# Kernel tuning notes

Measured on AMD Instinct MI355X. Metric: run time of the kernel, lower is better.

The kernel has to match this reference:

```python
import jax, jax.numpy as jnp
import numpy as np

N = 50000      # nodes
E = 800000     # edges (before self-loops)
F_IN = 128     # num_node_features
H = 128        # hidden_channels
G = 256        # graphs in batch
T = 4          # num_tasks


def setup_inputs() -> dict:
    key = jax.random.key(0)
    ks = jax.random.split(key, 12)
    x = jax.random.normal(ks[0], (N, F_IN), jnp.float32)
    edge_index = jax.random.randint(ks[1], (2, E), 0, N, dtype=jnp.int64)
    batch = jnp.sort(jax.random.randint(ks[2], (N,), 0, G, dtype=jnp.int64))
    s_in = 1.0 / np.sqrt(F_IN)
    s_h = 1.0 / np.sqrt(H)
    W1 = jax.random.normal(ks[3], (F_IN, H), jnp.float32) * s_in
    b1 = jnp.zeros((H,), jnp.float32)
    W2 = jax.random.normal(ks[4], (H, H), jnp.float32) * s_h
    b2 = jnp.zeros((H,), jnp.float32)
    Wfc = jax.random.normal(ks[5], (H, H), jnp.float32) * s_h
    bfc = jnp.zeros((H,), jnp.float32)
    Wh = jax.random.normal(ks[6], (T, H, 2), jnp.float32) * s_h
    bh = jnp.zeros((T, 2), jnp.float32)
    return {"x": x, "edge_index": edge_index, "batch": batch,
            "W1": W1, "b1": b1, "W2": W2, "b2": b2,
            "Wfc": Wfc, "bfc": bfc, "Wh": Wh, "bh": bh}


def _gcn_layer(x, W, b, src, dst, dinv):
    # GCNConv: out = D^{-1/2}(A+I)D^{-1/2} X W + b  (self-loops already in src/dst)
    h = x @ W                                    # [N, H] dense transform first (fewer edge features)
    coef = dinv[src] * dinv[dst]                 # [E+N] symmetric normalization
    msg = h[src] * coef[:, None]                 # [E+N, H] gathered messages
    out = jax.ops.segment_sum(msg, dst, num_segments=N)
    return out + b


def reference(x, edge_index, batch, W1, b1, W2, b2, Wfc, bfc, Wh, bh):
    loops = jnp.arange(N, dtype=edge_index.dtype)
    src = jnp.concatenate([edge_index[0], loops])  # [E+N]
    dst = jnp.concatenate([edge_index[1], loops])
    deg = jax.ops.segment_sum(jnp.ones_like(dst, dtype=x.dtype), dst, num_segments=N)
    dinv = jax.lax.rsqrt(deg)                      # deg >= 1 due to self-loops

    h = jax.nn.relu(_gcn_layer(x, W1, b1, src, dst, dinv))
    h = jax.nn.relu(_gcn_layer(h, W2, b2, src, dst, dinv))

    # global_mean_pool over batch ids
    sums = jax.ops.segment_sum(h, batch, num_segments=G)          # [G, H]
    cnt = jax.ops.segment_sum(jnp.ones((N,), h.dtype), batch, num_segments=G)
    pooled = sums / jnp.maximum(cnt, 1.0)[:, None]

    z = jax.nn.relu(pooled @ Wfc + bfc)                           # [G, H]
    out = jnp.einsum('gh,thc->tgc', z, Wh) + bh[:, None, :]       # [T, G, 2]
    return out
```

## Files before the change

### kernel.cpp

```cpp
#include <hip/hip_runtime.h>
#include <math.h>

constexpr int N = 50000;
constexpr int E = 800000;
constexpr int F = 128;
constexpr int G = 256;
constexpr int T = 4;

constexpr int BSH   = 5;
constexpr int BNODES= 1 << BSH;
constexpr int NBUCK = (N + BNODES - 1) / BNODES;
constexpr int CHUNK = 2048;
constexpr int NCHUNK= (E + CHUNK - 1) / CHUNK;
constexpr int SSH   = 13;

constexpr int WC_BLKS  = (F * F + 255) / 256;
constexpr int PRE_Z0   = 2 * WC_BLKS;
constexpr int PRE_ZB   = (G * F + 255) / 256;
constexpr int PRE_H0   = PRE_Z0 + PRE_ZB;
constexpr int PRE_BLKS = PRE_H0 + NCHUNK;

constexpr int GB1 = (N + 63) / 64;
constexpr int GCB = GB1 + NBUCK;
constexpr int AGB = N / 16;

typedef __attribute__((ext_vector_type(8))) short short8;
typedef __attribute__((ext_vector_type(4))) float floatx4;

__device__ inline float bf2f(unsigned short u) {
    union { unsigned int i; float f; } v;
    v.i = ((unsigned int)u) << 16;
    return v.f;
}
__device__ inline unsigned short f2bf(float f) {
    union { float f; unsigned int i; } v;
    v.f = f;
    unsigned int r = v.i + 0x7FFF + ((v.i >> 16) & 1);
    return (unsigned short)(r >> 16);
}
__device__ inline unsigned int pack2bf(float a, float b) {
    return (unsigned int)f2bf(a) | ((unsigned int)f2bf(b) << 16);
}

__device__ inline void wcast_one(const float* __restrict__ W,
                                 unsigned short* __restrict__ Whi,
                                 unsigned short* __restrict__ Wlo, int i) {
    if (i >= F * F) return;
    int k = i >> 7, n = i & 127;
    float w = W[i];
    unsigned short hi = f2bf(w);
    unsigned short lo = f2bf(w - bf2f(hi));
    int s = k >> 5, q = (k >> 3) & 3, j = k & 7;
    int idx = (((s * 128 + n) * 4 + q) * 8) + j;
    Whi[idx] = hi;
    Wlo[idx] = lo;
}

__global__ __launch_bounds__(256) void k_pre(const float* __restrict__ W1, const float* __restrict__ W2,
                                             unsigned short* __restrict__ w1h, unsigned short* __restrict__ w1l,
                                             unsigned short* __restrict__ w2h, unsigned short* __restrict__ w2l,
                                             const int* __restrict__ dst, int* __restrict__ cnts,
                                             float* __restrict__ pooled, int* __restrict__ ndeg) {
    __shared__ int h[NBUCK];
    int b = blockIdx.x, t = threadIdx.x;
    if (b < WC_BLKS) {
        wcast_one(W1, w1h, w1l, b * 256 + t);
    } else if (b < 2 * WC_BLKS) {
        wcast_one(W2, w2h, w2l, (b - WC_BLKS) * 256 + t);
    } else if (b < PRE_H0) {
        pooled[(b - PRE_Z0) * 256 + t] = 0.f;
    } else {
        int chunk = b - PRE_H0;
        for (int i = t; i < NBUCK; i += 256) h[i] = 0;
        __syncthreads();
        int base = chunk * CHUNK;
        for (int i = t; i < CHUNK; i += 256) {
            int e = base + i;
            if (e < E) {
                int d = dst[e];
                atomicAdd(&h[d >> BSH], 1);
                atomicAdd(&ndeg[d], 1);
            }
        }
        __syncthreads();
        for (int i = t; i < NBUCK; i += 256) cnts[chunk * NBUCK + i] = h[i];
    }
}

__global__ __launch_bounds__(256) void k_fillb(const int* __restrict__ src,
                                               const int* __restrict__ dst,
                                               const int* __restrict__ cnts,
                                               const int* __restrict__ btot,
                                               int* __restrict__ bucketbase,
                                               unsigned int* __restrict__ staging) {
    __shared__ int bb[NBUCK + 1];
    __shared__ int part[256];
    __shared__ int lofs[NBUCK];
    int chunk = blockIdx.x, t = threadIdx.x;

    constexpr int CH = (NBUCK + 255) / 256;
    int beg = t * CH;
    int end = (beg + CH < NBUCK) ? beg + CH : NBUCK;
    int tot[CH];
    int s = 0;
    for (int i = beg; i < end; ++i) {
        tot[i - beg] = btot[i];
        s += btot[i];
    }
    part[t] = s;
    __syncthreads();
    for (int off = 1; off < 256; off <<= 1) {
        int u = (t >= off) ? part[t - off] : 0;
        __syncthreads();
        part[t] += u;
        __syncthreads();
    }
    int run = (t == 0) ? 0 : part[t - 1];
    for (int i = beg; i < end; ++i) {
        bb[i] = run;
        run += tot[i - beg];
    }
    if (t == 255) bb[NBUCK] = part[255];
    __syncthreads();
    if (chunk == 0)
        for (int i = t; i <= NBUCK; i += 256) bucketbase[i] = bb[i];

    for (int i = t; i < NBUCK; i += 256)
        lofs[i] = bb[i] + cnts[chunk * NBUCK + i];
    __syncthreads();

    int base = chunk * CHUNK;
    for (int i = t; i < CHUNK; i += 256) {
        int e = base + i;
        if (e < E) {
            int d = dst[e];
            int pos = atomicAdd(&lofs[d >> BSH], 1);
            staging[pos] = (unsigned int)src[e] | ((unsigned int)(d & (BNODES - 1)) << 16);
        }
    }
}

__global__ __launch_bounds__(256) void k_passB(const unsigned int* __restrict__ staging,
                                               const int* __restrict__ bucketbase,
                                               int* __restrict__ csr,
                                               int* __restrict__ rowstart) {
    __shared__ unsigned int ent[1024];
    __shared__ int h[BNODES * 8], off_a[BNODES * 8];
    __shared__ int nodebase[BNODES], ndeg[BNODES];
    int b = blockIdx.x, t = threadIdx.x;
    int jb = bucketbase[b], je = bucketbase[b + 1];
    int M = je - jb;
    if (M > 1024) M = 1024;
    if (t < BNODES * 8) h[t] = 0;
    __syncthreads();

    for (int i = t; i < M; i += 256) {
        unsigned int en = staging[jb + i];
        ent[i] = en;
        int key = (((en >> 16) & (BNODES - 1)) << 3) | ((en & 0xFFFFu) >> SSH);
        atomicAdd(&h[key], 1);
    }
    __syncthreads();

    if (t < BNODES) {
        int s = 0;
#pragma unroll
        for (int c = 0; c < 8; ++c) s += h[t * 8 + c];
        ndeg[t] = s;
    }
    __syncthreads();
    if (t == 0) {
        int run = jb;
        for (int k = 0; k < BNODES; ++k) {
            nodebase[k] = run;
            run += ndeg[k];
        }
    }
    __syncthreads();
    if (t < BNODES) {
        int run = nodebase[t];
#pragma unroll
        for (int c = 0; c < 8; ++c) {
            off_a[t * 8 + c] = run;
            run += h[t * 8 + c];
        }
        int node = b * BNODES + t;
        if (node < N) rowstart[node] = nodebase[t];
    }
    if (b == 0 && t == 0) rowstart[N] = E;
    __syncthreads();

    for (int i = t; i < M; i += 256) {
        unsigned int en = ent[i];
        int key = (((en >> 16) & (BNODES - 1)) << 3) | ((en & 0xFFFFu) >> SSH);
        int loc = atomicAdd(&off_a[key], 1);
        csr[loc] = (int)(en & 0xFFFFu);
    }
}

template <bool ABF16>
__device__ __forceinline__ void gemm_body(const void* __restrict__ Ain,
                                          const unsigned short* __restrict__ Wph,
                                          const unsigned short* __restrict__ Wpl,
                                          const int* __restrict__ ndeg,
                                          float* __restrict__ dinvout,
                                          unsigned short* __restrict__ C16,
                                          int row0, int tid,
                                          unsigned short* __restrict__ Albs) {
    if (ABF16) {
        const uint4* A8 = (const uint4*)Ain;
        for (int f = tid; f < 64 * 16; f += 256) {
            int r = f >> 4, kq = f & 15;
            int row = row0 + r;
            uint4 v = make_uint4(0u, 0u, 0u, 0u);
            if (row < N) v = A8[row * 16 + kq];
            *(uint4*)&Albs[r * 136 + kq * 8] = v;
        }
    } else {
        const float4* A4 = (const float4*)Ain;
        for (int f = tid; f < 64 * 32; f += 256) {
            int r = f >> 5, kq = f & 31;
            int row = row0 + r;
            float4 v = make_float4(0.f, 0.f, 0.f, 0.f);
            if (row < N) v = A4[row * 32 + kq];
            ushort4 o;
            o.x = f2bf(v.x); o.y = f2bf(v.y); o.z = f2bf(v.z); o.w = f2bf(v.w);
            *(ushort4*)&Albs[r * 136 + kq * 4] = o;
        }
    }
    __syncthreads();

    int wv = tid >> 6;
    int lane = tid & 63;
    int c16 = lane & 15;
    int q = lane >> 4;
    int m = wv * 16 + c16;

    floatx4 acc[8];
#pragma unroll
    for (int nt = 0; nt < 8; ++nt) acc[nt] = (floatx4){0.f, 0.f, 0.f, 0.f};

    const short8* WH = (const short8*)Wph;
    const short8* WL = (const short8*)Wpl;
#pragma unroll
    for (int s = 0; s < 4; ++s) {
        short8 a = *(const short8*)&Albs[m * 136 + s * 32 + q * 8];
        int wb = s * 512 + c16 * 4 + q;
#pragma unroll
        for (int nt = 0; nt < 8; ++nt) {
            acc[nt] = __builtin_amdgcn_mfma_f32_16x16x32_bf16(a, WH[wb + nt * 64], acc[nt], 0, 0, 0);
            acc[nt] = __builtin_amdgcn_mfma_f32_16x16x32_bf16(a, WL[wb + nt * 64], acc[nt], 0, 0, 0);
        }
    }

    int rbase = row0 + wv * 16 + q * 4;
#pragma unroll
    for (int r = 0; r < 4; ++r) {
        int row = rbase + r;
        if (row < N) {
            float dv = rsqrtf((float)(ndeg[row] + 1));
            if (c16 == 0) dinvout[row] = dv;
#pragma unroll
            for (int nt = 0; nt < 8; ++nt)
                C16[row * 128 + nt * 16 + c16] = f2bf(acc[nt][r] * dv);
        }
    }
}

__global__ __launch_bounds__(256) void k_gemmcol(const float* __restrict__ x,
                                                 const unsigned short* __restrict__ w1h,
                                                 const unsigned short* __restrict__ w1l,
                                                 const int* __restrict__ ndeg,
                                                 float* __restrict__ dinv,
                                                 unsigned short* __restrict__ tmp16,
                                                 int* __restrict__ cnts,
                                                 int* __restrict__ btot) {
    __shared__ __align__(16) unsigned short Albs[64 * 136];
    int b = blockIdx.x, t = threadIdx.x;
    if (b < GB1) {
        gemm_body<false>(x, w1h, w1l, ndeg, dinv, tmp16, b * 64, t, Albs);
        return;
    }
    int j = b - GB1;
    int* part = (int*)Albs;
    int k0 = 2 * t, k1 = 2 * t + 1;
    int v0 = (k0 < NCHUNK) ? cnts[k0 * NBUCK + j] : 0;
    int v1 = (k1 < NCHUNK) ? cnts[k1 * NBUCK + j] : 0;
    int s = v0 + v1;
    part[t] = s;
    __syncthreads();
    for (int off = 1; off < 256; off <<= 1) {
        int u = (t >= off) ? part[t - off] : 0;
        __syncthreads();
        part[t] += u;
        __syncthreads();
    }
    int excl = part[t] - s;
    if (k0 < NCHUNK) cnts[k0 * NBUCK + j] = excl;
    if (k1 < NCHUNK) cnts[k1 * NBUCK + j] = excl + v0;
    if (t == 255) btot[j] = part[255];
}

__device__ inline void add8(const uint4& u, float* acc) {
    union { unsigned int i; float f; } a;
    a.i = u.x << 16;          acc[0] += a.f;
    a.i = u.x & 0xFFFF0000u;  acc[1] += a.f;
    a.i = u.y << 16;          acc[2] += a.f;
    a.i = u.y & 0xFFFF0000u;  acc[3] += a.f;
    a.i = u.z << 16;          acc[4] += a.f;
    a.i = u.z & 0xFFFF0000u;  acc[5] += a.f;
    a.i = u.w << 16;          acc[6] += a.f;
    a.i = u.w & 0xFFFF0000u;  acc[7] += a.f;
}

__device__ inline void fma8(const uint4& u, float c, float* acc) {
    union { unsigned int i; float f; } a;
    a.i = u.x << 16;          acc[0] = fmaf(a.f, c, acc[0]);
    a.i = u.x & 0xFFFF0000u;  acc[1] = fmaf(a.f, c, acc[1]);
    a.i = u.y << 16;          acc[2] = fmaf(a.f, c, acc[2]);
    a.i = u.y & 0xFFFF0000u;  acc[3] = fmaf(a.f, c, acc[3]);
    a.i = u.z << 16;          acc[4] = fmaf(a.f, c, acc[4]);
    a.i = u.z & 0xFFFF0000u;  acc[5] = fmaf(a.f, c, acc[5]);
    a.i = u.w << 16;          acc[6] = fmaf(a.f, c, acc[6]);
    a.i = u.w & 0xFFFF0000u;  acc[7] = fmaf(a.f, c, acc[7]);
}

__device__ __forceinline__ void agg_loop(const uint4* __restrict__ t8l,
                                         const int* __restrict__ csr,
                                         int jb, int je, float* acc) {
    int n8 = (je - jb) >> 3;
    int j = jb;
    if (n8 > 0) {
        int e[8];
#pragma unroll
        for (int k = 0; k < 8; ++k) e[k] = csr[j + k];
        for (int c = 0; c < n8; ++c) {
            uint4 u[8];
#pragma unroll
            for (int k = 0; k < 8; ++k) u[k] = t8l[e[k] * 16];
            j += 8;
            if (c + 1 < n8) {
#pragma unroll
                for (int k = 0; k < 8; ++k) e[k] = csr[j + k];
            }
#pragma unroll
            for (int k = 0; k < 8; ++k) add8(u[k], acc);
        }
    }
    if (j < je) {
        int e[8];
        float msk[8];
#pragma unroll
        for (int k = 0; k < 8; ++k) {
            int idx = j + k;
            e[k] = csr[idx < je ? idx : je - 1];
            msk[k] = (idx < je) ? 1.0f : 0.0f;
        }
        uint4 u[8];
#pragma unroll
        for (int k = 0; k < 8; ++k) u[k] = t8l[e[k] * 16];
#pragma unroll
        for (int k = 0; k < 8; ++k) fma8(u[k], msk[k], acc);
    }
}

__global__ __launch_bounds__(256) void k_agg1gemm(const unsigned short* __restrict__ tmp16,
                                                  const int* __restrict__ csr,
                                                  const int* __restrict__ rowstart,
                                                  const float* __restrict__ dinv,
                                                  const float* __restrict__ bias,
                                                  const unsigned short* __restrict__ w2h,
                                                  const unsigned short* __restrict__ w2l,
                                                  unsigned short* __restrict__ tmp2) {
    __shared__ __align__(16) unsigned short Albs[16 * 136];
    int tid = threadIdx.x;
    int row0 = blockIdx.x * 16;

    {
        int node = row0 + (tid >> 4);
        int lane = tid & 15;
        const uint4* t8l = (const uint4*)tmp16 + lane;
        float acc[8] = {0.f, 0.f, 0.f, 0.f, 0.f, 0.f, 0.f, 0.f};
        add8(t8l[node * 16], acc);
        agg_loop(t8l, csr, rowstart[node], rowstart[node + 1], acc);

        float di = dinv[node];
        const float4* b4 = (const float4*)bias;
        float4 ba = b4[lane * 2], bb = b4[lane * 2 + 1];
        uint4 o;
        o.x = pack2bf(fmaxf(fmaf(acc[0], di, ba.x), 0.f), fmaxf(fmaf(acc[1], di, ba.y), 0.f));
        o.y = pack2bf(fmaxf(fmaf(acc[2], di, ba.z), 0.f), fmaxf(fmaf(acc[3], di, ba.w), 0.f));
        o.z = pack2bf(fmaxf(fmaf(acc[4], di, bb.x), 0.f), fmaxf(fmaf(acc[5], di, bb.y), 0.f));
        o.w = pack2bf(fmaxf(fmaf(acc[6], di, bb.z), 0.f), fmaxf(fmaf(acc[7], di, bb.w), 0.f));
        *(uint4*)&Albs[(tid >> 4) * 136 + lane * 8] = o;
    }
    __syncthreads();

    int wv = tid >> 6;
    int lane = tid & 63;
    int c16 = lane & 15;
    int q = lane >> 4;

    floatx4 acc[2];
    acc[0] = (floatx4){0.f, 0.f, 0.f, 0.f};
    acc[1] = (floatx4){0.f, 0.f, 0.f, 0.f};

    const short8* WH = (const short8*)w2h;
    const short8* WL = (const short8*)w2l;
#pragma unroll
    for (int s = 0; s < 4; ++s) {
        short8 a = *(const short8*)&Albs[c16 * 136 + s * 32 + q * 8];
        int wb = s * 512 + c16 * 4 + q;
#pragma unroll
        for (int i = 0; i < 2; ++i) {
            int nt = wv * 2 + i;
            acc[i] = __builtin_amdgcn_mfma_f32_16x16x32_bf16(a, WH[wb + nt * 64], acc[i], 0, 0, 0);
            acc[i] = __builtin_amdgcn_mfma_f32_16x16x32_bf16(a, WL[wb + nt * 64], acc[i], 0, 0, 0);
        }
    }

    int rbase = row0 + q * 4;
#pragma unroll
    for (int r = 0; r < 4; ++r) {
        int row = rbase + r;
        float dv = dinv[row];
#pragma unroll
        for (int i = 0; i < 2; ++i) {
            int nt = wv * 2 + i;
            tmp2[row * 128 + nt * 16 + c16] = f2bf(acc[i][r] * dv);
        }
    }
}

__global__ __launch_bounds__(256) void k_agg(const unsigned short* __restrict__ tmp16,
                                             const int* __restrict__ csr,
                                             const int* __restrict__ rowstart,
                                             const float* __restrict__ dinv,
                                             const float* __restrict__ bias,
                                             const int* __restrict__ batch,
                                             float* __restrict__ pooled) {
    __shared__ float red[16][128];
    __shared__ int gid[16];
    int tid = threadIdx.x;
    int node0 = blockIdx.x * 16;
    int ns = tid >> 4, lane = tid & 15;
    int node = node0 + ns;
    const uint4* t8l = (const uint4*)tmp16 + lane;
    float acc[8] = {0.f, 0.f, 0.f, 0.f, 0.f, 0.f, 0.f, 0.f};
    add8(t8l[node * 16], acc);
    agg_loop(t8l, csr, rowstart[node], rowstart[node + 1], acc);

    float di = dinv[node];
    const float4* b4 = (const float4*)bias;
    float4 ba = b4[lane * 2], bb = b4[lane * 2 + 1];
    red[ns][lane * 8 + 0] = fmaxf(fmaf(acc[0], di, ba.x), 0.f);
    red[ns][lane * 8 + 1] = fmaxf(fmaf(acc[1], di, ba.y), 0.f);
    red[ns][lane * 8 + 2] = fmaxf(fmaf(acc[2], di, ba.z), 0.f);
    red[ns][lane * 8 + 3] = fmaxf(fmaf(acc[3], di, ba.w), 0.f);
    red[ns][lane * 8 + 4] = fmaxf(fmaf(acc[4], di, bb.x), 0.f);
    red[ns][lane * 8 + 5] = fmaxf(fmaf(acc[5], di, bb.y), 0.f);
    red[ns][lane * 8 + 6] = fmaxf(fmaf(acc[6], di, bb.z), 0.f);
    red[ns][lane * 8 + 7] = fmaxf(fmaf(acc[7], di, bb.w), 0.f);
    if (tid < 16) gid[tid] = batch[node0 + tid];
    __syncthreads();

    if (tid < 128) {
        int f = tid;
        float run = 0.f;
        int g = gid[0];
        for (int r = 0; r < 16; ++r) {
            if (gid[r] != g) {
                atomicAdd(&pooled[g * 128 + f], run);
                run = 0.f;
                g = gid[r];
            }
            run += red[r][f];
        }
        atomicAdd(&pooled[g * 128 + f], run);
    }
}

__global__ __launch_bounds__(128) void k_poolhead(const float* __restrict__ pooled,
                                                  const int* __restrict__ batch,
                                                  const float* __restrict__ Wfc,
                                                  const float* __restrict__ bfc,
                                                  const float* __restrict__ Wh,
                                                  const float* __restrict__ bh,
                                                  float* __restrict__ out) {
    __shared__ float p[128];
    __shared__ float zs[128];
    int g = blockIdx.x, t = threadIdx.x;

    int lo = 0, hi = N;
    while (lo < hi) { int m = (lo + hi) >> 1; if (batch[m] < g) lo = m + 1; else hi = m; }
    int lo1 = lo, hi1 = N;
    while (lo1 < hi1) { int m = (lo1 + hi1) >> 1; if (batch[m] < g + 1) lo1 = m + 1; else hi1 = m; }
    int cnt = lo1 - lo;
    float inv = 1.0f / (float)((cnt > 1) ? cnt : 1);

    p[t] = pooled[g * 128 + t] * inv;
    __syncthreads();

    float a = bfc[t];
    for (int k = 0; k < F; ++k) a = fmaf(p[k], Wfc[k * F + t], a);
    zs[t] = fmaxf(a, 0.f);
    __syncthreads();

    if (t < T * 2) {
        int task = t >> 1, c = t & 1;
        float a2 = bh[task * 2 + c];
        const float* wr = &Wh[task * F * 2 + c];
        for (int h = 0; h < F; ++h) a2 = fmaf(zs[h], wr[h * 2], a2);
        out[task * (G * 2) + g * 2 + c] = a2;
    }
}

extern "C" void kernel_launch(void* const* d_in, const int* in_sizes, int n_in,
                              void* d_out, int out_size, void* d_ws, size_t ws_size,
                              hipStream_t stream) {
    const float* x    = (const float*)d_in[0];
    const int*   ei   = (const int*)d_in[1];
    const int*   batch= (const int*)d_in[2];
    const float* W1   = (const float*)d_in[3];
    const float* b1   = (const float*)d_in[4];
    const float* W2   = (const float*)d_in[5];
    const float* b2   = (const float*)d_in[6];
    const float* Wfc  = (const float*)d_in[7];
    const float* bfc  = (const float*)d_in[8];
    const float* Wh   = (const float*)d_in[9];
    const float* bh   = (const float*)d_in[10];
    float* out = (float*)d_out;

    const int* srcp = ei;
    const int* dstp = ei + E;

    char* w = (char*)d_ws;
    auto alloc = [&](size_t bytes) {
        char* p = w;
        w += (bytes + 255) & ~(size_t)255;
        return p;
    };
    unsigned short* tmp16 = (unsigned short*)alloc((size_t)N * F * 2);
    unsigned short* tmp2  = (unsigned short*)alloc((size_t)N * F * 2);
    int*   csr      = (int*)  alloc((size_t)E * 4);
    unsigned int* staging = (unsigned int*)alloc((size_t)E * 4);
    int*   cnts     = (int*)  alloc((size_t)NCHUNK * NBUCK * 4);
    int*   btot     = (int*)  alloc((size_t)NBUCK * 4);
    int*   bucketbase=(int*)  alloc((size_t)(NBUCK + 1) * 4);
    int*   rowstart = (int*)  alloc((size_t)(N + 1) * 4);
    int*   ndeg     = (int*)  alloc((size_t)N * 4);
    float* dinv     = (float*)alloc((size_t)N * 4);
    float* pooled   = (float*)alloc((size_t)G * F * 4);
    unsigned short* w1h = (unsigned short*)alloc((size_t)F * F * 2);
    unsigned short* w1l = (unsigned short*)alloc((size_t)F * F * 2);
    unsigned short* w2h = (unsigned short*)alloc((size_t)F * F * 2);
    unsigned short* w2l = (unsigned short*)alloc((size_t)F * F * 2);

    hipMemsetAsync(ndeg, 0, (size_t)N * 4, stream);

    k_pre<<<PRE_BLKS, 256, 0, stream>>>(W1, W2, w1h, w1l, w2h, w2l, dstp, cnts, pooled, ndeg);

    k_gemmcol<<<GCB, 256, 0, stream>>>(x, w1h, w1l, ndeg, dinv, tmp16, cnts, btot);

    k_fillb<<<NCHUNK, 256, 0, stream>>>(srcp, dstp, cnts, btot, bucketbase, staging);
    k_passB<<<NBUCK, 256, 0, stream>>>(staging, bucketbase, csr, rowstart);

    k_agg1gemm<<<AGB, 256, 0, stream>>>(tmp16, csr, rowstart, dinv, b1, w2h, w2l, tmp2);

    k_agg<<<AGB, 256, 0, stream>>>(tmp2, csr, rowstart, dinv, b2, batch, pooled);

    k_poolhead<<<G, 128, 0, stream>>>(pooled, batch, Wfc, bfc, Wh, bh, out);
}
```

Measured before the change: 244.2 us.

## Derive degrees in passB instead of global atomics, rescale GEMM output there

Removes the per-edge global atomicAdd on ndeg in k_pre and the memset that cleared it. Node degrees are now computed in k_passB from the per-bucket shared histograms, which also write dinv. Because the first GEMM no longer knows dinv, k_passB re-reads and rescales each node's bf16 row of the GEMM output in place. This trades 800k global atomics for an extra read-modify-write pass over the 12.8MB tmp16 buffer and a second bf16 rounding of those values.

```diff
diff --git a/kernel.cpp b/kernel.cpp
--- a/kernel.cpp
+++ b/kernel.cpp
@@ -60,7 +60,7 @@
                                              unsigned short* __restrict__ w1h, unsigned short* __restrict__ w1l,
                                              unsigned short* __restrict__ w2h, unsigned short* __restrict__ w2l,
                                              const int* __restrict__ dst, int* __restrict__ cnts,
-                                             float* __restrict__ pooled, int* __restrict__ ndeg) {
+                                             float* __restrict__ pooled) {
     __shared__ int h[NBUCK];
     int b = blockIdx.x, t = threadIdx.x;
     if (b < WC_BLKS) {
@@ -76,11 +76,7 @@
         int base = chunk * CHUNK;
         for (int i = t; i < CHUNK; i += 256) {
             int e = base + i;
-            if (e < E) {
-                int d = dst[e];
-                atomicAdd(&h[d >> BSH], 1);
-                atomicAdd(&ndeg[d], 1);
-            }
+            if (e < E) atomicAdd(&h[dst[e] >> BSH], 1);
         }
         __syncthreads();
         for (int i = t; i < NBUCK; i += 256) cnts[chunk * NBUCK + i] = h[i];
@@ -143,10 +139,13 @@
 __global__ __launch_bounds__(256) void k_passB(const unsigned int* __restrict__ staging,
                                                const int* __restrict__ bucketbase,
                                                int* __restrict__ csr,
-                                               int* __restrict__ rowstart) {
+                                               int* __restrict__ rowstart,
+                                               float* __restrict__ dinv,
+                                               unsigned short* __restrict__ tmp16) {
     __shared__ unsigned int ent[1024];
     __shared__ int h[BNODES * 8], off_a[BNODES * 8];
     __shared__ int nodebase[BNODES], ndeg[BNODES];
+    __shared__ float sdinv[BNODES];
     int b = blockIdx.x, t = threadIdx.x;
     int jb = bucketbase[b], je = bucketbase[b + 1];
     int M = je - jb;
@@ -184,8 +183,13 @@
             off_a[t * 8 + c] = run;
             run += h[t * 8 + c];
         }
+        float dv = rsqrtf((float)(ndeg[t] + 1));
+        sdinv[t] = dv;
         int node = b * BNODES + t;
-        if (node < N) rowstart[node] = nodebase[t];
+        if (node < N) {
+            rowstart[node] = nodebase[t];
+            dinv[node] = dv;
+        }
     }
     if (b == 0 && t == 0) rowstart[N] = E;
     __syncthreads();
@@ -196,14 +200,28 @@
         int loc = atomicAdd(&off_a[key], 1);
         csr[loc] = (int)(en & 0xFFFFu);
     }
+
+    uint4* t4 = (uint4*)tmp16;
+    for (int i = t; i < BNODES * 16; i += 256) {
+        int rl = i >> 4, qi = i & 15;
+        int node = b * BNODES + rl;
+        if (node < N) {
+            float dv = sdinv[rl];
+            uint4 u = t4[node * 16 + qi];
+            uint4 o;
+            o.x = pack2bf(bf2f((unsigned short)(u.x & 0xFFFFu)) * dv, bf2f((unsigned short)(u.x >> 16)) * dv);
+            o.y = pack2bf(bf2f((unsigned short)(u.y & 0xFFFFu)) * dv, bf2f((unsigned short)(u.y >> 16)) * dv);
+            o.z = pack2bf(bf2f((unsigned short)(u.z & 0xFFFFu)) * dv, bf2f((unsigned short)(u.z >> 16)) * dv);
+            o.w = pack2bf(bf2f((unsigned short)(u.w & 0xFFFFu)) * dv, bf2f((unsigned short)(u.w >> 16)) * dv);
+            t4[node * 16 + qi] = o;
+        }
+    }
 }
 
 template <bool ABF16>
 __device__ __forceinline__ void gemm_body(const void* __restrict__ Ain,
                                           const unsigned short* __restrict__ Wph,
                                           const unsigned short* __restrict__ Wpl,
-                                          const int* __restrict__ ndeg,
-                                          float* __restrict__ dinvout,
                                           unsigned short* __restrict__ C16,
                                           int row0, int tid,
                                           unsigned short* __restrict__ Albs) {
@@ -258,11 +276,9 @@
     for (int r = 0; r < 4; ++r) {
         int row = rbase + r;
         if (row < N) {
-            float dv = rsqrtf((float)(ndeg[row] + 1));
-            if (c16 == 0) dinvout[row] = dv;
 #pragma unroll
             for (int nt = 0; nt < 8; ++nt)
-                C16[row * 128 + nt * 16 + c16] = f2bf(acc[nt][r] * dv);
+                C16[row * 128 + nt * 16 + c16] = f2bf(acc[nt][r]);
         }
     }
 }
@@ -270,15 +286,13 @@
 __global__ __launch_bounds__(256) void k_gemmcol(const float* __restrict__ x,
                                                  const unsigned short* __restrict__ w1h,
                                                  const unsigned short* __restrict__ w1l,
-                                                 const int* __restrict__ ndeg,
-                                                 float* __restrict__ dinv,
                                                  unsigned short* __restrict__ tmp16,
                                                  int* __restrict__ cnts,
                                                  int* __restrict__ btot) {
     __shared__ __align__(16) unsigned short Albs[64 * 136];
     int b = blockIdx.x, t = threadIdx.x;
     if (b < GB1) {
-        gemm_body<false>(x, w1h, w1l, ndeg, dinv, tmp16, b * 64, t, Albs);
+        gemm_body<false>(x, w1h, w1l, tmp16, b * 64, t, Albs);
         return;
     }
     int j = b - GB1;
@@ -548,7 +562,6 @@
     int*   btot     = (int*)  alloc((size_t)NBUCK * 4);
     int*   bucketbase=(int*)  alloc((size_t)(NBUCK + 1) * 4);
     int*   rowstart = (int*)  alloc((size_t)(N + 1) * 4);
-    int*   ndeg     = (int*)  alloc((size_t)N * 4);
     float* dinv     = (float*)alloc((size_t)N * 4);
     float* pooled   = (float*)alloc((size_t)G * F * 4);
     unsigned short* w1h = (unsigned short*)alloc((size_t)F * F * 2);
@@ -556,14 +569,12 @@
     unsigned short* w2h = (unsigned short*)alloc((size_t)F * F * 2);
     unsigned short* w2l = (unsigned short*)alloc((size_t)F * F * 2);
 
-    hipMemsetAsync(ndeg, 0, (size_t)N * 4, stream);
-
-    k_pre<<<PRE_BLKS, 256, 0, stream>>>(W1, W2, w1h, w1l, w2h, w2l, dstp, cnts, pooled, ndeg);
-
-    k_gemmcol<<<GCB, 256, 0, stream>>>(x, w1h, w1l, ndeg, dinv, tmp16, cnts, btot);
+    k_pre<<<PRE_BLKS, 256, 0, stream>>>(W1, W2, w1h, w1l, w2h, w2l, dstp, cnts, pooled);
+
+    k_gemmcol<<<GCB, 256, 0, stream>>>(x, w1h, w1l, tmp16, cnts, btot);
 
     k_fillb<<<NCHUNK, 256, 0, stream>>>(srcp, dstp, cnts, btot, bucketbase, staging);
-    k_passB<<<NBUCK, 256, 0, stream>>>(staging, bucketbase, csr, rowstart);
+    k_passB<<<NBUCK, 256, 0, stream>>>(staging, bucketbase, csr, rowstart, dinv, tmp16);
 
     k_agg1gemm<<<AGB, 256, 0, stream>>>(tmp16, csr, rowstart, dinv, b1, w2h, w2l, tmp2);
 
```

New measurement: 210.2 us. 13.9% less time.
